# Kernel tuning notes

Hardware: AMD Instinct MI355X
Metric: run time of the kernel (lower is better)

Reference implementation:

```python
import jax, jax.numpy as jnp
import numpy as np

B, T, INPUT_DIM = 4, 2048, 256
D_MODEL = 512                       # hidden_dim // 2
EXPAND = 2
D_INNER = D_MODEL * EXPAND          # 1024
HEADDIM = 128                       # _pick_headdim(1024)
NHEADS = D_INNER // HEADDIM         # 8
DSTATE = 16
DCONV = 4
NLAYERS = 4
CONV_DIM = D_INNER + 2 * DSTATE            # 1056
D_IN_PROJ = 2 * D_INNER + 2 * DSTATE + NHEADS  # 2088
EPS = 1e-5


def _dir_params(key):
    ks = jax.random.split(key, 5)
    return dict(
        in_w=jax.random.normal(ks[0], (NLAYERS, D_IN_PROJ, D_MODEL)) * 0.02,
        conv_w=jax.random.normal(ks[1], (NLAYERS, CONV_DIM, DCONV)) * 0.1,
        conv_b=jnp.zeros((NLAYERS, CONV_DIM)),
        dt_bias=jnp.log(jnp.expm1(jax.random.uniform(ks[2], (NLAYERS, NHEADS), minval=1e-3, maxval=0.1))),
        A_log=jnp.log(jax.random.uniform(ks[3], (NLAYERS, NHEADS), minval=1.0, maxval=16.0)),
        D=jnp.ones((NLAYERS, NHEADS)),
        rms_w=jnp.ones((NLAYERS, D_INNER)),
        out_w=jax.random.normal(ks[4], (NLAYERS, D_MODEL, D_INNER)) * 0.02,
    )


def setup_inputs():
    key = jax.random.key(0)
    kx, ke, kf, kb = jax.random.split(key, 4)
    inp = {
        "x": jax.random.normal(kx, (B, T, INPUT_DIM), dtype=jnp.float32),
        "embed_w": jax.random.normal(ke, (D_MODEL, INPUT_DIM)) * 0.02,
        "embed_b": jnp.zeros((D_MODEL,)),
        "ln1_w": jnp.ones((D_MODEL,)), "ln1_b": jnp.zeros((D_MODEL,)),
        "lnout_w": jnp.ones((2 * D_MODEL,)), "lnout_b": jnp.zeros((2 * D_MODEL,)),
    }
    for tag, p in (("f", _dir_params(kf)), ("b", _dir_params(kb))):
        for k, v in p.items():
            inp[f"{k}_{tag}"] = v
    return inp


def _silu(x):
    return x * jax.nn.sigmoid(x)


def _layernorm(x, w, b):
    m = jnp.mean(x, -1, keepdims=True)
    v = jnp.mean((x - m) ** 2, -1, keepdims=True)
    return (x - m) * jax.lax.rsqrt(v + EPS) * w + b


def _mamba2(h, in_w, conv_w, conv_b, dt_bias, A_log, Dh, rms_w, out_w):
    """One Mamba2 (SSD) block: in_proj -> causal depthwise conv -> selective scan
    -> gated RMSNorm -> out_proj. Sequential scan is math-equivalent to the
    chunked SSD kernel."""
    Bb, Tt, _ = h.shape
    zxbcdt = jnp.einsum('btd,ed->bte', h, in_w)
    z = zxbcdt[..., :D_INNER]
    xBC = zxbcdt[..., D_INNER:D_INNER + CONV_DIM]
    dt = zxbcdt[..., D_INNER + CONV_DIM:]                      # [B,T,H]
    # causal depthwise conv over time (kernel DCONV), then silu
    xc = jax.lax.conv_general_dilated(
        jnp.transpose(xBC, (0, 2, 1)), conv_w[:, None, :], (1,),
        [(DCONV - 1, 0)], feature_group_count=CONV_DIM)
    xBC = _silu(jnp.transpose(xc, (0, 2, 1)) + conv_b)
    xs = xBC[..., :D_INNER].reshape(Bb, Tt, NHEADS, HEADDIM)   # [B,T,H,P]
    Bm = xBC[..., D_INNER:D_INNER + DSTATE]                    # [B,T,N]
    Cm = xBC[..., D_INNER + DSTATE:]                           # [B,T,N]
    dt = jax.nn.softplus(dt + dt_bias)                         # [B,T,H]
    dA = jnp.exp(dt * (-jnp.exp(A_log)))                       # [B,T,H]
    xdt = xs * dt[..., None]                                   # [B,T,H,P]
    tm = lambda a: jnp.moveaxis(a, 1, 0)                       # time-major

    def step(s, inp):
        dA_t, xdt_t, B_t, C_t = inp
        s = dA_t[:, :, None, None] * s + xdt_t[..., None] * B_t[:, None, None, :]
        return s, jnp.einsum('bhpn,bn->bhp', s, C_t)

    s0 = jnp.zeros((Bb, NHEADS, HEADDIM, DSTATE), h.dtype)
    _, ys = jax.lax.scan(step, s0, (tm(dA), tm(xdt), tm(Bm), tm(Cm)))
    y = jnp.moveaxis(ys, 0, 1) + Dh[None, None, :, None] * xs
    y = y.reshape(Bb, Tt, D_INNER)
    g = y * _silu(z)                                           # gated RMSNorm (norm after gate)
    g = g * jax.lax.rsqrt(jnp.mean(g * g, -1, keepdims=True) + EPS) * rms_w
    return jnp.einsum('bti,oi->bto', g, out_w)


def _forward(x, embed_w, embed_b, ln1_w, ln1_b, lnout_w, lnout_b,
             in_w_f, conv_w_f, conv_b_f, dt_bias_f, A_log_f, D_f, rms_w_f, out_w_f,
             in_w_b, conv_w_b, conv_b_b, dt_bias_b, A_log_b, D_b, rms_w_b, out_w_b):
    h = _layernorm(jnp.einsum('bti,oi->bto', x, embed_w) + embed_b, ln1_w, ln1_b)
    h_f, h_b = h, h[:, ::-1]
    for i in range(NLAYERS):
        h_f = _mamba2(h_f, in_w_f[i], conv_w_f[i], conv_b_f[i], dt_bias_f[i],
                      A_log_f[i], D_f[i], rms_w_f[i], out_w_f[i]) + h_f
    for i in range(NLAYERS):
        h_b = _mamba2(h_b, in_w_b[i], conv_w_b[i], conv_b_b[i], dt_bias_b[i],
                      A_log_b[i], D_b[i], rms_w_b[i], out_w_b[i]) + h_b
    out = jnp.concatenate([h_f, h_b[:, ::-1]], axis=-1)        # [B,T,2*D_MODEL]
    return _layernorm(out, lnout_w, lnout_b)


def reference(x, embed_w, embed_b, ln1_w, ln1_b, lnout_w, lnout_b,
              in_w_f, conv_w_f, conv_b_f, dt_bias_f, A_log_f, D_f, rms_w_f, out_w_f,
              in_w_b, conv_w_b, conv_b_b, dt_bias_b, A_log_b, D_b, rms_w_b, out_w_b):
    return _forward(x, embed_w, embed_b, ln1_w, ln1_b, lnout_w, lnout_b,
                    in_w_f, conv_w_f, conv_b_f, dt_bias_f, A_log_f, D_f, rms_w_f, out_w_f,
                    in_w_b, conv_w_b, conv_b_b, dt_bias_b, A_log_b, D_b, rms_w_b, out_w_b)
```

## Files before the change

kernel.cpp:

```cpp
#include <hip/hip_runtime.h>
#include <hip/hip_bf16.h>
#include <math.h>

#define BB 4
#define TT 2048
#define BT 8192
#define DM 512
#define DI 1024
#define NH 8
#define HD 128
#define DS 16
#define CONVD 1056
#define DPROJ 2088
#define NL 4
#define CL 128
#define NCH 16
#define NE 131072

typedef __hip_bfloat16 bf16;
typedef __attribute__((ext_vector_type(8))) short short8;
typedef __attribute__((ext_vector_type(4))) short short4v;
typedef __attribute__((ext_vector_type(4))) float f32x4;

#define AS_G __attribute__((address_space(1)))
#define AS_L __attribute__((address_space(3)))

static __device__ __forceinline__ float b2f_raw(short v){
  union { unsigned u; float f; } c; c.u = ((unsigned)(unsigned short)v) << 16; return c.f;
}

static __device__ __forceinline__ void red2(float& a, float& b, float* sb){
  #pragma unroll
  for (int o = 32; o; o >>= 1){ a += __shfl_down(a, o); b += __shfl_down(b, o); }
  int w = threadIdx.x >> 6;
  if ((threadIdx.x & 63) == 0){ sb[w] = a; sb[4+w] = b; }
  __syncthreads();
  a = sb[0]+sb[1]+sb[2]+sb[3];
  b = sb[4]+sb[5]+sb[6]+sb[7];
}

__global__ __launch_bounds__(256) void detect_dtype(const void* x, int* flagp){
  __shared__ int cnt;
  if (threadIdx.x == 0) cnt = 0;
  __syncthreads();
  const bf16* p = (const bf16*)x;
  int bad = 0;
  for (int i = threadIdx.x; i < 32768; i += 256){
    float v = __bfloat162float(p[i]);
    if (!isfinite(v) || fabsf(v) > 1e4f) bad++;
  }
  atomicAdd(&cnt, bad);
  __syncthreads();
  if (threadIdx.x == 0) *flagp = (cnt > 100) ? 1 : 0;
}

__global__ __launch_bounds__(256) void convert_in(const void* src, bf16* dst, int n,
                                                  const int* flagp){
  int f = *flagp;
  for (int i = blockIdx.x*256 + threadIdx.x; i < n; i += gridDim.x*256){
    if (f) dst[i] = __float2bfloat16(((const float*)src)[i]);
    else   dst[i] = ((const bf16*)src)[i];
  }
}

template<int OP>
__global__ __launch_bounds__(256) void gemm_nt(
    const bf16* __restrict__ A, const bf16* __restrict__ W0, const bf16* __restrict__ W1,
    bf16* C, const bf16* X, float* aux,
    int M, int N, int K, int lda, long sA, long sC)
{
  const int z = blockIdx.z;
  const bf16* Az = A + (long)z * sA;
  const bf16* W = z ? W1 : W0;
  const int m0 = blockIdx.x * 128, n0 = blockIdx.y * 128;
  __shared__ __align__(16) bf16 As[128*32];
  __shared__ __align__(16) bf16 Bs[128*32];
  const int tid  = threadIdx.x;
  const int lane = tid & 63, wv = tid >> 6;
  const int wm = wv >> 1, wn = wv & 1;
  const int quad = lane >> 4, l16 = lane & 15;
  const int srow = lane >> 2;
  const int skb  = (lane & 3) * 16;

  f32x4 acc[4][4];
  #pragma unroll
  for (int i=0;i<4;i++)
    #pragma unroll
    for (int j=0;j<4;j++) acc[i][j] = (f32x4){0.f,0.f,0.f,0.f};

  for (int k0 = 0; k0 < K; k0 += 32){
    __syncthreads();
    #pragma unroll
    for (int is = 0; is < 2; ++is){
      int r = is*64 + wv*16 + srow;
      const char* gA = (const char*)(Az + (long)(m0 + r)*lda + k0) + skb;
      char* lA = (char*)As + (long)(is*64 + wv*16)*64;
      __builtin_amdgcn_global_load_lds((const AS_G void*)gA, (AS_L void*)lA, 16, 0, 0);
      int rn = n0 + r; rn = rn < N ? rn : N-1;
      const char* gB = (const char*)(W + (long)rn*K + k0) + skb;
      char* lB = (char*)Bs + (long)(is*64 + wv*16)*64;
      __builtin_amdgcn_global_load_lds((const AS_G void*)gB, (AS_L void*)lB, 16, 0, 0);
    }
    __syncthreads();
    short8 af[4], bfr[4];
    #pragma unroll
    for (int mi=0;mi<4;mi++) af[mi]  = *(const short8*)((const char*)As + (long)(wm*64+mi*16+l16)*64 + quad*16);
    #pragma unroll
    for (int ni=0;ni<4;ni++) bfr[ni] = *(const short8*)((const char*)Bs + (long)(wn*64+ni*16+l16)*64 + quad*16);
    #pragma unroll
    for (int mi=0;mi<4;mi++)
      #pragma unroll
      for (int ni=0;ni<4;ni++)
        acc[mi][ni] = __builtin_amdgcn_mfma_f32_16x16x32_bf16(af[mi], bfr[ni], acc[mi][ni], 0, 0, 0);
  }

  bf16* Cz = C + (long)z * sC;
  const bf16* Xz = (OP==2) ? (X + (long)z * sC) : X;
  #pragma unroll
  for (int mi=0;mi<4;mi++){
    #pragma unroll
    for (int ni=0;ni<4;ni++){
      #pragma unroll
      for (int r=0;r<4;r++){
        int row = m0 + wm*64 + mi*16 + quad*4 + r;
        int col = n0 + wn*64 + ni*16 + l16;
        if (col < N){
          float v = acc[mi][ni][r];
          if (OP==1) v += __bfloat162float(X[col]);
          if (OP==2) v += __bfloat162float(Xz[(long)row*N + col]);
          Cz[(long)row*N + col] = __float2bfloat16(v);
          if (OP==3 && col >= DPROJ-8)
            aux[(long)z*BT*8 + (long)row*8 + (col-(DPROJ-8))] = v;
        }
      }
    }
  }
}

__global__ __launch_bounds__(256) void embed_ln(const bf16* __restrict__ hp,
    const bf16* __restrict__ w, const bf16* __restrict__ bb, bf16* __restrict__ h)
{
  __shared__ float sb[8];
  int bt = blockIdx.x; int b = bt >> 11, t = bt & 2047;
  const bf16* r = hp + (long)bt*DM;
  int c0 = threadIdx.x, c1 = threadIdx.x + 256;
  float v0 = __bfloat162float(r[c0]);
  float v1 = __bfloat162float(r[c1]);
  float s = v0+v1, ss = v0*v0+v1*v1;
  red2(s, ss, sb);
  float m = s / DM;
  float var = ss / DM - m*m;
  float rs = rsqrtf(fmaxf(var, 0.f) + 1e-5f);
  float a0 = (v0-m)*rs*__bfloat162float(w[c0]) + __bfloat162float(bb[c0]);
  float a1 = (v1-m)*rs*__bfloat162float(w[c1]) + __bfloat162float(bb[c1]);
  bf16* o0 = h + (long)bt*DM;
  bf16* o1 = h + ((long)BT + (long)b*TT + (TT-1-t)) * DM;
  o0[c0] = __float2bfloat16(a0); o0[c1] = __float2bfloat16(a1);
  o1[c0] = __float2bfloat16(a0); o1[c1] = __float2bfloat16(a1);
}

__global__ __launch_bounds__(256) void conv_silu(const bf16* __restrict__ zx,
    const bf16* __restrict__ cw0, const bf16* __restrict__ cw1,
    const bf16* __restrict__ cb0, const bf16* __restrict__ cb1,
    bf16* __restrict__ xbc)
{
  int bt = blockIdx.x, dir = blockIdx.y;
  int t = bt & 2047;
  const bf16* cw = dir ? cw1 : cw0;
  const bf16* cb = dir ? cb1 : cb0;
  const bf16* zr = zx + ((long)dir*BT + bt)*DPROJ + DI;
  bf16* orow = xbc + ((long)dir*BT + bt)*CONVD;
  for (int cg = threadIdx.x; cg < CONVD/4; cg += 256){
    int c = cg*4;
    short8 w01 = *(const short8*)(cw + c*4);
    short8 w23 = *(const short8*)(cw + c*4 + 8);
    short4v bi = *(const short4v*)(cb + c);
    float acc[4];
    #pragma unroll
    for (int k=0;k<4;k++) acc[k] = b2f_raw(bi[k]);
    #pragma unroll
    for (int j=0;j<4;j++){
      if (t - 3 + j >= 0){
        short4v xv = *(const short4v*)(zr + (long)(j-3)*DPROJ + c);
        acc[0] = fmaf(b2f_raw(w01[j]),   b2f_raw(xv[0]), acc[0]);
        acc[1] = fmaf(b2f_raw(w01[4+j]), b2f_raw(xv[1]), acc[1]);
        acc[2] = fmaf(b2f_raw(w23[j]),   b2f_raw(xv[2]), acc[2]);
        acc[3] = fmaf(b2f_raw(w23[4+j]), b2f_raw(xv[3]), acc[3]);
      }
    }
    short4v ov;
    #pragma unroll
    for (int k=0;k<4;k++){
      float sg = 1.f / (1.f + expf(-acc[k]));
      ov[k] = (short)__bfloat16_as_ushort(__float2bfloat16(acc[k] * sg));
    }
    *(short4v*)(orow + c) = ov;
  }
}

__global__ __launch_bounds__(256) void dt_kernel(const float* __restrict__ draw,
    const bf16* __restrict__ db0, const bf16* __restrict__ db1,
    const bf16* __restrict__ al0, const bf16* __restrict__ al1,
    float2* __restrict__ dadt)
{
  int idx = blockIdx.x*256 + threadIdx.x;
  int dir = idx >> 16, r = idx & 65535;
  int bt = r >> 3, h = r & 7;
  int b = bt >> 11, t = bt & 2047;
  float x = draw[idx] + __bfloat162float((dir?db1:db0)[h]);
  float sp = (x > 20.f) ? x : log1pf(expf(x));
  float a = expf(-expf(__bfloat162float((dir?al1:al0)[h])) * sp);
  long o = (((long)dir*BB + b)*NH + h)*TT + t;
  float2 v; v.x = a; v.y = sp;
  dadt[o] = v;
}

#define SC_LOAD(X,BV,CV,DD,T0) do{ \
  _Pragma("unroll") \
  for (int _i=0;_i<4;_i++){ \
    const bf16* _rr = xr + (long)((T0)+_i)*CONVD; \
    X[_i]  = __bfloat162float(_rr[h*HD + p]); \
    BV[_i] = *(const short8*)(_rr + DI + half*8); \
    CV[_i] = *(const short8*)(_rr + DI + DS + half*8); \
    DD[_i] = ddr[(T0)+_i]; \
  } }while(0)

#define SC_STEP(X,BV,CV,DD,T0) do{ \
  _Pragma("unroll") \
  for (int _i=0;_i<4;_i++){ \
    float _dav = DD[_i].x, _dtv = DD[_i].y; \
    float _xdt = X[_i] * _dtv; \
    float _acc = 0.f; \
    _Pragma("unroll") \
    for (int _n=0;_n<8;_n++){ \
      s[_n] = fmaf(_dav, s[_n], _xdt * b2f_raw(BV[_i][_n])); \
      _acc  = fmaf(s[_n], b2f_raw(CV[_i][_n]), _acc); } \
    _acc += __shfl_xor(_acc, 1); \
    if (!half) xw[(long)((T0)+_i)*CONVD + h*HD + p] = __float2bfloat16(_acc + Dv*X[_i]); \
  } }while(0)

#define CH_LOAD(X,BV,DD,T0) do{ \
  _Pragma("unroll") \
  for (int _i=0;_i<4;_i++){ \
    const bf16* _rr = xr + (long)((T0)+_i)*CONVD; \
    X[_i]  = __bfloat162float(_rr[h*HD + p]); \
    BV[_i] = *(const short8*)(_rr + DI + half*8); \
    DD[_i] = ddr[(T0)+_i]; \
  } }while(0)

#define CH_STEP(X,BV,DD) do{ \
  _Pragma("unroll") \
  for (int _i=0;_i<4;_i++){ \
    float _dav = DD[_i].x, _dtv = DD[_i].y; \
    float _xdt = X[_i] * _dtv; \
    _Pragma("unroll") \
    for (int _n=0;_n<8;_n++) \
      s[_n] = fmaf(_dav, s[_n], _xdt * b2f_raw(BV[_i][_n])); \
    pacc *= _dav; \
  } }while(0)

__global__ __launch_bounds__(256) void chunk_local(const bf16* __restrict__ xbc,
    const float2* __restrict__ dadt, float* __restrict__ SC, float* __restrict__ Pc)
{
  int c = blockIdx.x, dbh = blockIdx.y;
  int dir = dbh >> 5, b = (dbh >> 3) & 3, h = dbh & 7;
  int tid = threadIdx.x, p = tid >> 1, half = tid & 1;
  const bf16* xr = xbc + ((long)dir*BT + (long)b*TT) * CONVD;
  const float2* ddr = dadt + (((long)dir*BB + b)*NH + h)*TT;
  float s[8];
  #pragma unroll
  for (int n=0;n<8;n++) s[n] = 0.f;
  float pacc = 1.f;
  const int c0 = c*CL;

  float xA[4], xB2[4];
  short8 BA[4], BB2[4];
  float2 dA_[4], dB_[4];

  CH_LOAD(xA,BA,dA_, c0);
  for (int t0 = c0; t0 < c0+CL; t0 += 8){
    CH_LOAD(xB2,BB2,dB_, t0+4);
    CH_STEP(xA,BA,dA_);
    if (t0+8 < c0+CL) CH_LOAD(xA,BA,dA_, t0+8);
    CH_STEP(xB2,BB2,dB_);
  }
  long e = (long)dbh*2048 + p*16 + half*8;
  #pragma unroll
  for (int n=0;n<8;n++) SC[(long)c*NE + e + n] = s[n];
  if (tid == 0) Pc[dbh*NCH + c] = pacc;
}

__global__ __launch_bounds__(256) void chunk_combine(float* __restrict__ SC,
    const float* __restrict__ Pc)
{
  int e = blockIdx.x*256 + threadIdx.x;
  int dbh = e >> 11;
  float s = 0.f;
  #pragma unroll
  for (int c=0;c<NCH;c++){
    float tmp = SC[(long)c*NE + e];
    SC[(long)c*NE + e] = s;
    s = Pc[dbh*NCH + c]*s + tmp;
  }
}

__global__ __launch_bounds__(256) void chunk_apply(bf16* __restrict__ xbc,
    const float2* __restrict__ dadt, const float* __restrict__ SC,
    const bf16* __restrict__ D0, const bf16* __restrict__ D1)
{
  int c = blockIdx.x, dbh = blockIdx.y;
  int dir = dbh >> 5, b = (dbh >> 3) & 3, h = dbh & 7;
  int tid = threadIdx.x, p = tid >> 1, half = tid & 1;
  const bf16* xr = xbc + ((long)dir*BT + (long)b*TT) * CONVD;
  bf16* xw = xbc + ((long)dir*BT + (long)b*TT) * CONVD;
  const float2* ddr = dadt + (((long)dir*BB + b)*NH + h)*TT;
  float Dv = __bfloat162float(dir ? D1[h] : D0[h]);
  long e = (long)dbh*2048 + p*16 + half*8;
  float s[8];
  #pragma unroll
  for (int n=0;n<8;n++) s[n] = SC[(long)c*NE + e + n];
  const int c0 = c*CL;

  float xA[4], xB2[4];
  short8 BA[4], BB2[4], CA[4], CB2[4];
  float2 dA_[4], dB_[4];

  SC_LOAD(xA,BA,CA,dA_, c0);
  for (int t0 = c0; t0 < c0+CL; t0 += 8){
    SC_LOAD(xB2,BB2,CB2,dB_, t0+4);
    SC_STEP(xA,BA,CA,dA_, t0);
    if (t0+8 < c0+CL) SC_LOAD(xA,BA,CA,dA_, t0+8);
    SC_STEP(xB2,BB2,CB2,dB_, t0+4);
  }
}

__global__ __launch_bounds__(256) void gate_rms(const bf16* __restrict__ xbc, bf16* zx,
    const bf16* __restrict__ rw0, const bf16* __restrict__ rw1)
{
  __shared__ float sb[8];
  int bt = blockIdx.x, dir = blockIdx.y;
  const bf16* yr = xbc + ((long)dir*BT + bt)*CONVD;
  bf16* zr = zx + ((long)dir*BT + bt)*DPROJ;
  const bf16* rw = dir ? rw1 : rw0;
  int c = threadIdx.x*4;
  short4v yv4 = *(const short4v*)(yr + c);
  short4v zv4 = *(const short4v*)(zr + c);
  short4v rw4 = *(const short4v*)(rw + c);
  float gv[4], ss = 0.f, dummy = 0.f;
  #pragma unroll
  for (int k=0;k<4;k++){
    float yv = b2f_raw(yv4[k]);
    float zv = b2f_raw(zv4[k]);
    float sg = 1.f/(1.f+expf(-zv));
    gv[k] = yv * zv * sg;
    ss += gv[k]*gv[k];
  }
  red2(ss, dummy, sb);
  float sc = rsqrtf(ss / DI + 1e-5f);
  short4v ov;
  #pragma unroll
  for (int k=0;k<4;k++)
    ov[k] = (short)__bfloat16_as_ushort(__float2bfloat16(gv[k]*sc*b2f_raw(rw4[k])));
  *(short4v*)(zr + c) = ov;
}

__global__ __launch_bounds__(256) void final_ln(const bf16* __restrict__ h,
    const bf16* __restrict__ lw, const bf16* __restrict__ lb, void* out,
    int mode, const int* flagp)
{
  __shared__ float sb[8];
  int bt = blockIdx.x; int b = bt >> 11, t = bt & 2047;
  int f32out = mode ? *flagp : 0;
  const bf16* rf = h + (long)bt*DM;
  const bf16* rb = h + ((long)BT + (long)b*TT + (TT-1-t))*DM;
  float v[4], s = 0.f, ss = 0.f;
  #pragma unroll
  for (int i=0;i<4;i++){
    int c = threadIdx.x + i*256;
    v[i] = __bfloat162float(c < DM ? rf[c] : rb[c-DM]);
    s += v[i]; ss += v[i]*v[i];
  }
  red2(s, ss, sb);
  float m = s / (2*DM);
  float var = ss / (2*DM) - m*m;
  float rs = rsqrtf(fmaxf(var, 0.f) + 1e-5f);
  #pragma unroll
  for (int i=0;i<4;i++){
    int c = threadIdx.x + i*256;
    float o = (v[i]-m)*rs*__bfloat162float(lw[c]) + __bfloat162float(lb[c]);
    if (f32out) ((float*)out)[(long)bt*(2*DM) + c] = o;
    else        ((bf16*)out)[(long)bt*(2*DM) + c] = __float2bfloat16(o);
  }
}

extern "C" void kernel_launch(void* const* d_in, const int* in_sizes, int n_in,
                              void* d_out, int out_size, void* d_ws, size_t ws_size,
                              hipStream_t stream)
{
  char* wsp = (char*)d_ws;
  auto take = [&](size_t bytes){ char* p = wsp; wsp += (bytes + 63) & ~(size_t)63; return p; };
  int*   flagp = (int*)  take(4);
  bf16*  h     = (bf16*) take((size_t)2*BT*DM*2);
  bf16*  zx    = (bf16*) take((size_t)2*BT*DPROJ*2);
  bf16*  xbc   = (bf16*) take((size_t)2*BT*CONVD*2);
  float2* dadt = (float2*)take((size_t)2*BB*NH*TT*8);
  float* draw  = (float*)take((size_t)2*BT*NH*4);
  float* Pc    = (float*)take((size_t)64*NCH*4);
  float* SC    = (float*)take((size_t)NCH*NE*4);
  size_t needDirect = (size_t)(wsp - (char*)d_ws);

  static const int cnt[23] = {
    BT*256, DM*256, DM, DM, DM, 2*DM, 2*DM,
    NL*DPROJ*DM, NL*CONVD*4, NL*CONVD, NL*NH, NL*NH, NL*NH, NL*DI, NL*DM*DI,
    NL*DPROJ*DM, NL*CONVD*4, NL*CONVD, NL*NH, NL*NH, NL*NH, NL*DI, NL*DM*DI };
  bf16* canon[23];
  for (int i = 0; i < 23; ++i) canon[i] = (bf16*)take((size_t)cnt[i]*2);
  size_t needFull = (size_t)(wsp - (char*)d_ws);

  const int convMode = (ws_size >= needFull) ? 1 : 0;

  const bf16* in[23];
  if (convMode){
    detect_dtype<<<1,256,0,stream>>>(d_in[0], flagp);
    for (int i = 0; i < 23; ++i){
      int grid = (cnt[i] + 255)/256; if (grid > 2048) grid = 2048;
      convert_in<<<grid,256,0,stream>>>(d_in[i], canon[i], cnt[i], flagp);
      in[i] = canon[i];
    }
  } else {
    for (int i = 0; i < 23; ++i) in[i] = (const bf16*)d_in[i];
  }

  const bf16* x       = in[0];
  const bf16* embed_w = in[1];
  const bf16* embed_b = in[2];
  const bf16* ln1_w   = in[3];
  const bf16* ln1_b   = in[4];
  const bf16* lnout_w = in[5];
  const bf16* lnout_b = in[6];
  const bf16* in_w[2]   = {in[7],  in[15]};
  const bf16* conv_w[2] = {in[8],  in[16]};
  const bf16* conv_b[2] = {in[9],  in[17]};
  const bf16* dt_b[2]   = {in[10], in[18]};
  const bf16* A_log[2]  = {in[11], in[19]};
  const bf16* Dp[2]     = {in[12], in[20]};
  const bf16* rms_w[2]  = {in[13], in[21]};
  const bf16* out_w[2]  = {in[14], in[22]};

  bf16* hpre = xbc;

  gemm_nt<1><<<dim3(64,4,1),256,0,stream>>>(x, embed_w, embed_w, hpre, embed_b, nullptr,
                                            BT, DM, 256, 256, 0, 0);
  embed_ln<<<dim3(BT),256,0,stream>>>(hpre, ln1_w, ln1_b, h);

  for (int i = 0; i < NL; ++i){
    gemm_nt<3><<<dim3(64,17,2),256,0,stream>>>(h, in_w[0]+(size_t)i*DPROJ*DM, in_w[1]+(size_t)i*DPROJ*DM,
        zx, nullptr, draw, BT, DPROJ, DM, DM, (long)BT*DM, (long)BT*DPROJ);
    conv_silu<<<dim3(BT,2),256,0,stream>>>(zx, conv_w[0]+(size_t)i*CONVD*4, conv_w[1]+(size_t)i*CONVD*4,
        conv_b[0]+(size_t)i*CONVD, conv_b[1]+(size_t)i*CONVD, xbc);
    dt_kernel<<<dim3(512),256,0,stream>>>(draw, dt_b[0]+i*NH, dt_b[1]+i*NH,
        A_log[0]+i*NH, A_log[1]+i*NH, dadt);
    chunk_local<<<dim3(NCH,64),256,0,stream>>>(xbc, dadt, SC, Pc);
    chunk_combine<<<dim3(NE/256),256,0,stream>>>(SC, Pc);
    chunk_apply<<<dim3(NCH,64),256,0,stream>>>(xbc, dadt, SC, Dp[0]+i*NH, Dp[1]+i*NH);
    gate_rms<<<dim3(BT,2),256,0,stream>>>(xbc, zx, rms_w[0]+(size_t)i*DI, rms_w[1]+(size_t)i*DI);
    gemm_nt<2><<<dim3(64,4,2),256,0,stream>>>(zx, out_w[0]+(size_t)i*DM*DI, out_w[1]+(size_t)i*DM*DI,
        h, h, nullptr, BT, DM, DI, DPROJ, (long)BT*DPROJ, (long)BT*DM);
  }

  final_ln<<<dim3(BT),256,0,stream>>>(h, lnout_w, lnout_b, d_out, convMode, flagp);
  (void)needDirect; (void)in_sizes; (void)n_in; (void)out_size;
}
```

Measured before the change: 1.237 ms.

## Remap SSD scan to one wave per head and use taller in-proj GEMM tiles

The chunked scan kernels now give each 64-lane wave one (dir,batch,head) and each lane two head-dim channels with all 16 state entries. This drops the half-lane split and its shuffle reduction, loads x as packed bf16 pairs, and writes outputs as packed pairs. The grid shrinks to 4 heads per block, and the per-lane state grows to 32 floats, which raises register pressure. The in-projection GEMM switches to a 256-row M tile with an 8-fragment N loop per wave to reuse B tiles more, trading fewer blocks for more accumulators per thread.

```diff
diff --git a/kernel.cpp b/kernel.cpp
--- a/kernel.cpp
+++ b/kernel.cpp
@@ -28,6 +28,17 @@
 static __device__ __forceinline__ float b2f_raw(short v){
   union { unsigned u; float f; } c; c.u = ((unsigned)(unsigned short)v) << 16; return c.f;
 }
+static __device__ __forceinline__ float u32_lo(unsigned u){
+  union { unsigned u; float f; } c; c.u = u << 16; return c.f;
+}
+static __device__ __forceinline__ float u32_hi(unsigned u){
+  union { unsigned u; float f; } c; c.u = u & 0xffff0000u; return c.f;
+}
+static __device__ __forceinline__ unsigned pack_bf16x2(float a, float b){
+  unsigned lo = __bfloat16_as_ushort(__float2bfloat16(a));
+  unsigned hi = __bfloat16_as_ushort(__float2bfloat16(b));
+  return lo | (hi << 16);
+}
 
 static __device__ __forceinline__ void red2(float& a, float& b, float* sb){
   #pragma unroll
@@ -63,54 +74,60 @@
   }
 }
 
-template<int OP>
-__global__ __launch_bounds__(256) void gemm_nt(
+template<int OP, int MR>
+__global__ __launch_bounds__(256,2) void gemm_nt(
     const bf16* __restrict__ A, const bf16* __restrict__ W0, const bf16* __restrict__ W1,
     bf16* C, const bf16* X, float* aux,
     int M, int N, int K, int lda, long sA, long sC)
 {
+  constexpr int NF = (MR == 256) ? 8 : 4;
   const int z = blockIdx.z;
   const bf16* Az = A + (long)z * sA;
   const bf16* W = z ? W1 : W0;
-  const int m0 = blockIdx.x * 128, n0 = blockIdx.y * 128;
-  __shared__ __align__(16) bf16 As[128*32];
+  const int m0 = blockIdx.x * MR, n0 = blockIdx.y * 128;
+  __shared__ __align__(16) bf16 As[MR*32];
   __shared__ __align__(16) bf16 Bs[128*32];
   const int tid  = threadIdx.x;
   const int lane = tid & 63, wv = tid >> 6;
-  const int wm = wv >> 1, wn = wv & 1;
+  const int wmB = (MR == 256) ? wv*64 : (wv >> 1)*64;
+  const int wnB = (MR == 256) ? 0     : (wv & 1)*64;
   const int quad = lane >> 4, l16 = lane & 15;
   const int srow = lane >> 2;
   const int skb  = (lane & 3) * 16;
 
-  f32x4 acc[4][4];
+  f32x4 acc[4][NF];
   #pragma unroll
   for (int i=0;i<4;i++)
     #pragma unroll
-    for (int j=0;j<4;j++) acc[i][j] = (f32x4){0.f,0.f,0.f,0.f};
+    for (int j=0;j<NF;j++) acc[i][j] = (f32x4){0.f,0.f,0.f,0.f};
 
   for (int k0 = 0; k0 < K; k0 += 32){
     __syncthreads();
     #pragma unroll
-    for (int is = 0; is < 2; ++is){
+    for (int is = 0; is < MR/64; ++is){
       int r = is*64 + wv*16 + srow;
       const char* gA = (const char*)(Az + (long)(m0 + r)*lda + k0) + skb;
       char* lA = (char*)As + (long)(is*64 + wv*16)*64;
       __builtin_amdgcn_global_load_lds((const AS_G void*)gA, (AS_L void*)lA, 16, 0, 0);
+    }
+    #pragma unroll
+    for (int is = 0; is < 2; ++is){
+      int r = is*64 + wv*16 + srow;
       int rn = n0 + r; rn = rn < N ? rn : N-1;
       const char* gB = (const char*)(W + (long)rn*K + k0) + skb;
       char* lB = (char*)Bs + (long)(is*64 + wv*16)*64;
       __builtin_amdgcn_global_load_lds((const AS_G void*)gB, (AS_L void*)lB, 16, 0, 0);
     }
     __syncthreads();
-    short8 af[4], bfr[4];
-    #pragma unroll
-    for (int mi=0;mi<4;mi++) af[mi]  = *(const short8*)((const char*)As + (long)(wm*64+mi*16+l16)*64 + quad*16);
-    #pragma unroll
-    for (int ni=0;ni<4;ni++) bfr[ni] = *(const short8*)((const char*)Bs + (long)(wn*64+ni*16+l16)*64 + quad*16);
+    short8 af[4], bfr[NF];
+    #pragma unroll
+    for (int mi=0;mi<4;mi++)  af[mi]  = *(const short8*)((const char*)As + (long)(wmB+mi*16+l16)*64 + quad*16);
+    #pragma unroll
+    for (int ni=0;ni<NF;ni++) bfr[ni] = *(const short8*)((const char*)Bs + (long)(wnB+ni*16+l16)*64 + quad*16);
     #pragma unroll
     for (int mi=0;mi<4;mi++)
       #pragma unroll
-      for (int ni=0;ni<4;ni++)
+      for (int ni=0;ni<NF;ni++)
         acc[mi][ni] = __builtin_amdgcn_mfma_f32_16x16x32_bf16(af[mi], bfr[ni], acc[mi][ni], 0, 0, 0);
   }
 
@@ -119,11 +136,11 @@
   #pragma unroll
   for (int mi=0;mi<4;mi++){
     #pragma unroll
-    for (int ni=0;ni<4;ni++){
+    for (int ni=0;ni<NF;ni++){
       #pragma unroll
       for (int r=0;r<4;r++){
-        int row = m0 + wm*64 + mi*16 + quad*4 + r;
-        int col = n0 + wn*64 + ni*16 + l16;
+        int row = m0 + wmB + mi*16 + quad*4 + r;
+        int col = n0 + wnB + ni*16 + l16;
         if (col < N){
           float v = acc[mi][ni][r];
           if (OP==1) v += __bfloat162float(X[col]);
@@ -215,79 +232,100 @@
   dadt[o] = v;
 }
 
-#define SC_LOAD(X,BV,CV,DD,T0) do{ \
+#define CLG_LOAD(G, T0) do{ \
   _Pragma("unroll") \
   for (int _i=0;_i<4;_i++){ \
     const bf16* _rr = xr + (long)((T0)+_i)*CONVD; \
-    X[_i]  = __bfloat162float(_rr[h*HD + p]); \
-    BV[_i] = *(const short8*)(_rr + DI + half*8); \
-    CV[_i] = *(const short8*)(_rr + DI + DS + half*8); \
-    DD[_i] = ddr[(T0)+_i]; \
+    G##x[_i]  = *(const unsigned*)(_rr + xoff); \
+    G##B0[_i] = *(const short8*)(_rr + DI); \
+    G##B1[_i] = *(const short8*)(_rr + DI + 8); \
+    G##d[_i]  = ddr[(T0)+_i]; \
   } }while(0)
 
-#define SC_STEP(X,BV,CV,DD,T0) do{ \
+#define CLG_STEP(G) do{ \
   _Pragma("unroll") \
   for (int _i=0;_i<4;_i++){ \
-    float _dav = DD[_i].x, _dtv = DD[_i].y; \
-    float _xdt = X[_i] * _dtv; \
-    float _acc = 0.f; \
+    float _da = G##d[_i].x, _dt = G##d[_i].y; \
+    float _x0 = u32_lo(G##x[_i]), _x1 = u32_hi(G##x[_i]); \
+    float _xd0 = _x0*_dt, _xd1 = _x1*_dt; \
     _Pragma("unroll") \
     for (int _n=0;_n<8;_n++){ \
-      s[_n] = fmaf(_dav, s[_n], _xdt * b2f_raw(BV[_i][_n])); \
-      _acc  = fmaf(s[_n], b2f_raw(CV[_i][_n]), _acc); } \
-    _acc += __shfl_xor(_acc, 1); \
-    if (!half) xw[(long)((T0)+_i)*CONVD + h*HD + p] = __float2bfloat16(_acc + Dv*X[_i]); \
+      float _b = b2f_raw(G##B0[_i][_n]); \
+      s0[_n] = fmaf(_da, s0[_n], _xd0*_b); \
+      s1[_n] = fmaf(_da, s1[_n], _xd1*_b); \
+      float _b2 = b2f_raw(G##B1[_i][_n]); \
+      s0[8+_n] = fmaf(_da, s0[8+_n], _xd0*_b2); \
+      s1[8+_n] = fmaf(_da, s1[8+_n], _xd1*_b2); \
+    } \
+    pacc *= _da; \
   } }while(0)
 
-#define CH_LOAD(X,BV,DD,T0) do{ \
+#define CAG_LOAD(G, T0) do{ \
   _Pragma("unroll") \
   for (int _i=0;_i<4;_i++){ \
     const bf16* _rr = xr + (long)((T0)+_i)*CONVD; \
-    X[_i]  = __bfloat162float(_rr[h*HD + p]); \
-    BV[_i] = *(const short8*)(_rr + DI + half*8); \
-    DD[_i] = ddr[(T0)+_i]; \
+    G##x[_i]  = *(const unsigned*)(_rr + xoff); \
+    G##B0[_i] = *(const short8*)(_rr + DI); \
+    G##B1[_i] = *(const short8*)(_rr + DI + 8); \
+    G##C0[_i] = *(const short8*)(_rr + DI + DS); \
+    G##C1[_i] = *(const short8*)(_rr + DI + DS + 8); \
+    G##d[_i]  = ddr[(T0)+_i]; \
   } }while(0)
 
-#define CH_STEP(X,BV,DD) do{ \
+#define CAG_STEP(G, T0) do{ \
   _Pragma("unroll") \
   for (int _i=0;_i<4;_i++){ \
-    float _dav = DD[_i].x, _dtv = DD[_i].y; \
-    float _xdt = X[_i] * _dtv; \
+    float _da = G##d[_i].x, _dt = G##d[_i].y; \
+    float _x0 = u32_lo(G##x[_i]), _x1 = u32_hi(G##x[_i]); \
+    float _xd0 = _x0*_dt, _xd1 = _x1*_dt; \
+    float _a0 = 0.f, _a1 = 0.f; \
     _Pragma("unroll") \
-    for (int _n=0;_n<8;_n++) \
-      s[_n] = fmaf(_dav, s[_n], _xdt * b2f_raw(BV[_i][_n])); \
-    pacc *= _dav; \
+    for (int _n=0;_n<8;_n++){ \
+      float _b = b2f_raw(G##B0[_i][_n]); \
+      float _c = b2f_raw(G##C0[_i][_n]); \
+      s0[_n] = fmaf(_da, s0[_n], _xd0*_b); \
+      s1[_n] = fmaf(_da, s1[_n], _xd1*_b); \
+      _a0 = fmaf(s0[_n], _c, _a0); \
+      _a1 = fmaf(s1[_n], _c, _a1); \
+      float _b2 = b2f_raw(G##B1[_i][_n]); \
+      float _c2 = b2f_raw(G##C1[_i][_n]); \
+      s0[8+_n] = fmaf(_da, s0[8+_n], _xd0*_b2); \
+      s1[8+_n] = fmaf(_da, s1[8+_n], _xd1*_b2); \
+      _a0 = fmaf(s0[8+_n], _c2, _a0); \
+      _a1 = fmaf(s1[8+_n], _c2, _a1); \
+    } \
+    *(unsigned*)(xw + (long)((T0)+_i)*CONVD + xoff) = \
+        pack_bf16x2(_a0 + Dv*_x0, _a1 + Dv*_x1); \
   } }while(0)
 
-__global__ __launch_bounds__(256) void chunk_local(const bf16* __restrict__ xbc,
+__global__ __launch_bounds__(256,1) void chunk_local(const bf16* __restrict__ xbc,
     const float2* __restrict__ dadt, float* __restrict__ SC, float* __restrict__ Pc)
 {
-  int c = blockIdx.x, dbh = blockIdx.y;
+  int c = blockIdx.x;
+  int dbh = blockIdx.y*4 + (threadIdx.x >> 6);
+  int lane = threadIdx.x & 63;
   int dir = dbh >> 5, b = (dbh >> 3) & 3, h = dbh & 7;
-  int tid = threadIdx.x, p = tid >> 1, half = tid & 1;
   const bf16* xr = xbc + ((long)dir*BT + (long)b*TT) * CONVD;
-  const float2* ddr = dadt + (((long)dir*BB + b)*NH + h)*TT;
-  float s[8];
-  #pragma unroll
-  for (int n=0;n<8;n++) s[n] = 0.f;
+  const float2* ddr = dadt + (long)dbh*TT;
+  const int xoff = h*HD + lane*2;
+  float s0[16], s1[16];
+  #pragma unroll
+  for (int n=0;n<16;n++){ s0[n]=0.f; s1[n]=0.f; }
   float pacc = 1.f;
   const int c0 = c*CL;
 
-  float xA[4], xB2[4];
-  short8 BA[4], BB2[4];
-  float2 dA_[4], dB_[4];
-
-  CH_LOAD(xA,BA,dA_, c0);
+  unsigned Ax[4], Bx[4]; short8 AB0[4], AB1[4], BB0[4], BB1[4]; float2 Ad[4], Bd[4];
+  CLG_LOAD(A, c0);
   for (int t0 = c0; t0 < c0+CL; t0 += 8){
-    CH_LOAD(xB2,BB2,dB_, t0+4);
-    CH_STEP(xA,BA,dA_);
-    if (t0+8 < c0+CL) CH_LOAD(xA,BA,dA_, t0+8);
-    CH_STEP(xB2,BB2,dB_);
-  }
-  long e = (long)dbh*2048 + p*16 + half*8;
-  #pragma unroll
-  for (int n=0;n<8;n++) SC[(long)c*NE + e + n] = s[n];
-  if (tid == 0) Pc[dbh*NCH + c] = pacc;
+    CLG_LOAD(B, t0+4);
+    CLG_STEP(A);
+    if (t0+8 < c0+CL) CLG_LOAD(A, t0+8);
+    CLG_STEP(B);
+  }
+  float* sc = SC + (long)c*NE + (long)dbh*2048 + lane*32;
+  #pragma unroll
+  for (int n=0;n<16;n++){ sc[n] = s0[n]; sc[16+n] = s1[n]; }
+  if (lane == 0) Pc[dbh*NCH + c] = pacc;
 }
 
 __global__ __launch_bounds__(256) void chunk_combine(float* __restrict__ SC,
@@ -304,33 +342,34 @@
   }
 }
 
-__global__ __launch_bounds__(256) void chunk_apply(bf16* __restrict__ xbc,
+__global__ __launch_bounds__(256,1) void chunk_apply(bf16* __restrict__ xbc,
     const float2* __restrict__ dadt, const float* __restrict__ SC,
     const bf16* __restrict__ D0, const bf16* __restrict__ D1)
 {
-  int c = blockIdx.x, dbh = blockIdx.y;
+  int c = blockIdx.x;
+  int dbh = blockIdx.y*4 + (threadIdx.x >> 6);
+  int lane = threadIdx.x & 63;
   int dir = dbh >> 5, b = (dbh >> 3) & 3, h = dbh & 7;
-  int tid = threadIdx.x, p = tid >> 1, half = tid & 1;
   const bf16* xr = xbc + ((long)dir*BT + (long)b*TT) * CONVD;
   bf16* xw = xbc + ((long)dir*BT + (long)b*TT) * CONVD;
-  const float2* ddr = dadt + (((long)dir*BB + b)*NH + h)*TT;
+  const float2* ddr = dadt + (long)dbh*TT;
+  const int xoff = h*HD + lane*2;
   float Dv = __bfloat162float(dir ? D1[h] : D0[h]);
-  long e = (long)dbh*2048 + p*16 + half*8;
-  float s[8];
-  #pragma unroll
-  for (int n=0;n<8;n++) s[n] = SC[(long)c*NE + e + n];
+  const float* sc = SC + (long)c*NE + (long)dbh*2048 + lane*32;
+  float s0[16], s1[16];
+  #pragma unroll
+  for (int n=0;n<16;n++){ s0[n] = sc[n]; s1[n] = sc[16+n]; }
   const int c0 = c*CL;
 
-  float xA[4], xB2[4];
-  short8 BA[4], BB2[4], CA[4], CB2[4];
-  float2 dA_[4], dB_[4];
-
-  SC_LOAD(xA,BA,CA,dA_, c0);
+  unsigned Ax[4], Bx[4];
+  short8 AB0[4], AB1[4], BB0[4], BB1[4], AC0[4], AC1[4], BC0[4], BC1[4];
+  float2 Ad[4], Bd[4];
+  CAG_LOAD(A, c0);
   for (int t0 = c0; t0 < c0+CL; t0 += 8){
-    SC_LOAD(xB2,BB2,CB2,dB_, t0+4);
-    SC_STEP(xA,BA,CA,dA_, t0);
-    if (t0+8 < c0+CL) SC_LOAD(xA,BA,CA,dA_, t0+8);
-    SC_STEP(xB2,BB2,CB2,dB_, t0+4);
+    CAG_LOAD(B, t0+4);
+    CAG_STEP(A, t0);
+    if (t0+8 < c0+CL) CAG_LOAD(A, t0+8);
+    CAG_STEP(B, t0+4);
   }
 }
 
@@ -449,22 +488,22 @@
 
   bf16* hpre = xbc;
 
-  gemm_nt<1><<<dim3(64,4,1),256,0,stream>>>(x, embed_w, embed_w, hpre, embed_b, nullptr,
+  gemm_nt<1,128><<<dim3(64,4,1),256,0,stream>>>(x, embed_w, embed_w, hpre, embed_b, nullptr,
                                             BT, DM, 256, 256, 0, 0);
   embed_ln<<<dim3(BT),256,0,stream>>>(hpre, ln1_w, ln1_b, h);
 
   for (int i = 0; i < NL; ++i){
-    gemm_nt<3><<<dim3(64,17,2),256,0,stream>>>(h, in_w[0]+(size_t)i*DPROJ*DM, in_w[1]+(size_t)i*DPROJ*DM,
+    gemm_nt<3,256><<<dim3(32,17,2),256,0,stream>>>(h, in_w[0]+(size_t)i*DPROJ*DM, in_w[1]+(size_t)i*DPROJ*DM,
         zx, nullptr, draw, BT, DPROJ, DM, DM, (long)BT*DM, (long)BT*DPROJ);
     conv_silu<<<dim3(BT,2),256,0,stream>>>(zx, conv_w[0]+(size_t)i*CONVD*4, conv_w[1]+(size_t)i*CONVD*4,
         conv_b[0]+(size_t)i*CONVD, conv_b[1]+(size_t)i*CONVD, xbc);
     dt_kernel<<<dim3(512),256,0,stream>>>(draw, dt_b[0]+i*NH, dt_b[1]+i*NH,
         A_log[0]+i*NH, A_log[1]+i*NH, dadt);
-    chunk_local<<<dim3(NCH,64),256,0,stream>>>(xbc, dadt, SC, Pc);
+    chunk_local<<<dim3(NCH,16),256,0,stream>>>(xbc, dadt, SC, Pc);
     chunk_combine<<<dim3(NE/256),256,0,stream>>>(SC, Pc);
-    chunk_apply<<<dim3(NCH,64),256,0,stream>>>(xbc, dadt, SC, Dp[0]+i*NH, Dp[1]+i*NH);
+    chunk_apply<<<dim3(NCH,16),256,0,stream>>>(xbc, dadt, SC, Dp[0]+i*NH, Dp[1]+i*NH);
     gate_rms<<<dim3(BT,2),256,0,stream>>>(xbc, zx, rms_w[0]+(size_t)i*DI, rms_w[1]+(size_t)i*DI);
-    gemm_nt<2><<<dim3(64,4,2),256,0,stream>>>(zx, out_w[0]+(size_t)i*DM*DI, out_w[1]+(size_t)i*DM*DI,
+    gemm_nt<2,128><<<dim3(64,4,2),256,0,stream>>>(zx, out_w[0]+(size_t)i*DM*DI, out_w[1]+(size_t)i*DM*DI,
         h, h, nullptr, BT, DM, DI, DPROJ, (long)BT*DPROJ, (long)BT*DM);
   }
 
```

Measured after the change: 1.212 ms. -2.0%, faster.
